# Kernel tuning notes

Hardware: AMD Instinct MI355X
Metric: run time of the kernel (lower is better)

The kernel has to match this reference:

```python
import jax, jax.numpy as jnp
import numpy as np

HIDDEN = 2048
INTER = 1408
N_ROUTED = 32
N_SHARED = 2
TOP_K = 6
B, S = 2, 1024


def setup_inputs() -> dict:
    key = jax.random.key(0)
    ks = jax.random.split(key, 9)
    scale = 0.02
    x = jax.random.normal(ks[0], (B, S, HIDDEN), dtype=jnp.float32)
    w_router = jax.random.normal(ks[1], (HIDDEN, N_ROUTED), dtype=jnp.float32) * scale
    wg = jax.random.normal(ks[2], (N_ROUTED, HIDDEN, INTER), dtype=jnp.float32) * scale
    wu = jax.random.normal(ks[3], (N_ROUTED, HIDDEN, INTER), dtype=jnp.float32) * scale
    wd = jax.random.normal(ks[4], (N_ROUTED, INTER, HIDDEN), dtype=jnp.float32) * scale
    sg = jax.random.normal(ks[5], (N_SHARED, HIDDEN, INTER), dtype=jnp.float32) * scale
    su = jax.random.normal(ks[6], (N_SHARED, HIDDEN, INTER), dtype=jnp.float32) * scale
    sd = jax.random.normal(ks[7], (N_SHARED, INTER, HIDDEN), dtype=jnp.float32) * scale
    return {"x": x, "w_router": w_router, "wg": wg, "wu": wu, "wd": wd,
            "sg": sg, "su": su, "sd": sd}


def _swiglu(xf, wg_e, wu_e, wd_e):
    # xf: [T, D]; wg_e/wu_e: [D, F]; wd_e: [F, D]
    h = jax.nn.silu(xf @ wg_e) * (xf @ wu_e)
    return h @ wd_e


def reference(x, w_router, wg, wu, wd, sg, su, sd):
    Bb, Ss, D = x.shape
    xf = x.reshape(-1, D)                      # [T, D], T = B*S
    T = xf.shape[0]

    # Shared experts: applied densely to every token, summed.
    shared = jnp.zeros_like(xf)
    for i in range(sg.shape[0]):               # small fixed count (2)
        shared = shared + _swiglu(xf, sg[i], su[i], sd[i])

    # Router: softmax over all routed experts, then top-k + renormalize.
    probs = jax.nn.softmax(xf @ w_router, axis=-1)            # [T, E]
    topw, topi = jax.lax.top_k(probs, TOP_K)                  # [T, K]
    topw = topw / jnp.sum(topw, axis=-1, keepdims=True)

    # Dense [T, E] combine weights (zero where expert not selected).
    E = wg.shape[0]
    wdense = jnp.zeros((T, E), dtype=xf.dtype)
    wdense = wdense.at[jnp.arange(T)[:, None], topi].add(topw)

    # Scan over experts, accumulating weighted expert outputs (memory-light).
    def body(acc, ew):
        wg_e, wu_e, wd_e, w_e = ew            # w_e: [T] combine weight for this expert
        y = _swiglu(xf, wg_e, wu_e, wd_e)     # [T, D]
        return acc + w_e[:, None] * y, None

    routed, _ = jax.lax.scan(body, jnp.zeros_like(xf), (wg, wu, wd, wdense.T))

    return (shared + routed).reshape(Bb, Ss, D)
```

## Files before the change

### kernel.cpp

```cpp
#include <hip/hip_runtime.h>
#include <hip/hip_bf16.h>

#define T_TOK 2048
#define D_HID 2048
#define F_INT 1408
#define N_EXP 32
#define TOPK 6
#define NJOBS 34
#define SH_BASE 12288
#define ROWS_TOTAL 16384
#define MAXT_GU 159
#define GU_NBN 22
#define MAXT_DN 159
#define LDSW 40

typedef __bf16 bf16;
typedef __bf16 bf16x4 __attribute__((ext_vector_type(4)));
typedef __bf16 bf16x8 __attribute__((ext_vector_type(8)));
typedef float f32x4 __attribute__((ext_vector_type(4)));

#define BAR() asm volatile("s_waitcnt lgkmcnt(0)\n\ts_barrier" ::: "memory")

__device__ __forceinline__ int swz16(int r, int k) {
    return r * LDSW + ((((k >> 3) ^ ((r >> 3) & 3) ^ ((r >> 5) & 3)) & 3) << 3) + (k & 7);
}

__device__ __forceinline__ int decode_tile(const int* __restrict__ counts, int bid,
                                           int NBN, int MSH, int NSH,
                                           int& job, int& n0, int& m0) {
    int total = 0;
    for (int j = 0; j < NJOBS; ++j) {
        int c = (j < N_EXP) ? counts[j] : T_TOK;
        total += ((c + (1 << MSH) - 1) >> MSH) * NBN;
    }
    if (bid >= total) return 0;
    int q = total >> 3, r = total & 7, x = bid & 7, o = bid >> 3;
    int L = (x < r ? x * (q + 1) : r * (q + 1) + (x - r) * q) + o;
    int acc = 0;
    for (int j = 0; j < NJOBS; ++j) {
        int c = (j < N_EXP) ? counts[j] : T_TOK;
        int tc = (c + (1 << MSH) - 1) >> MSH;
        int b = tc * NBN;
        if (L < acc + b) {
            int rem = L - acc;
            int n0i = rem / tc;
            job = j;
            n0 = n0i << NSH;
            m0 = (rem - n0i * tc) << MSH;
            return 1;
        }
        acc += b;
    }
    return 0;
}

__global__ __launch_bounds__(256) void k_xcvt(const float* __restrict__ x,
                                              bf16* __restrict__ xb) {
    int i = blockIdx.x * 2048 + threadIdx.x * 8;
    float4 f0 = *(const float4*)(x + i);
    float4 f1 = *(const float4*)(x + i + 4);
    bf16x8 v = {(bf16)f0.x, (bf16)f0.y, (bf16)f0.z, (bf16)f0.w,
                (bf16)f1.x, (bf16)f1.y, (bf16)f1.z, (bf16)f1.w};
    *(bf16x8*)(xb + i) = v;
}

__global__ __launch_bounds__(256) void k_router(const float* __restrict__ x,
                                                const float* __restrict__ wr,
                                                int* __restrict__ counts,
                                                int* __restrict__ tok_e,
                                                float* __restrict__ tok_w) {
    int t = blockIdx.x;
    int tid = threadIdx.x;
    __shared__ float xs[D_HID];
    __shared__ float part[8][32];
    __shared__ float probs[N_EXP];

    const float4* xsrc = (const float4*)(x + (size_t)t * D_HID);
    float4* xdst = (float4*)xs;
    for (int i = tid; i < D_HID / 4; i += 256) xdst[i] = xsrc[i];
    __syncthreads();

    int e = tid & 31, c = tid >> 5;
    float p = 0.f;
    const float* wp = wr + e;
    #pragma unroll 8
    for (int h = c * 256; h < c * 256 + 256; ++h) p += xs[h] * wp[h * 32];
    part[c][e] = p;
    __syncthreads();

    if (tid < 32) {
        float l = 0.f;
        #pragma unroll
        for (int cc = 0; cc < 8; ++cc) l += part[cc][tid];
        float m = l;
        for (int off = 16; off; off >>= 1) m = fmaxf(m, __shfl_xor(m, off));
        float ex = __expf(l - m);
        float s = ex;
        for (int off = 16; off; off >>= 1) s += __shfl_xor(s, off);
        probs[tid] = ex / s;
    }
    __syncthreads();

    if (tid == 0) {
        unsigned used = 0;
        int ids[TOPK]; float wsv[TOPK]; float wsum = 0.f;
        for (int k = 0; k < TOPK; ++k) {
            int best = 0; float bv = -1.f;
            for (int ee = 0; ee < N_EXP; ++ee)
                if (!((used >> ee) & 1u) && probs[ee] > bv) { bv = probs[ee]; best = ee; }
            used |= 1u << best;
            ids[k] = best; wsv[k] = bv; wsum += bv;
        }
        float inv = 1.f / wsum;
        for (int k = 0; k < TOPK; ++k) {
            tok_e[t * TOPK + k] = ids[k];
            tok_w[t * TOPK + k] = wsv[k] * inv;
            atomicAdd(&counts[ids[k]], 1);
        }
    }
}

__global__ void k_plan(const int* __restrict__ counts, int* __restrict__ offs,
                       int* __restrict__ cursors) {
    int tid = threadIdx.x;
    if (tid < N_EXP) cursors[tid] = 0;
    if (tid == 0) {
        int o = 0;
        offs[0] = 0;
        for (int e2 = 0; e2 < N_EXP; ++e2) { o += counts[e2]; offs[e2 + 1] = o; }
        offs[33] = offs[32] + T_TOK;
        offs[34] = offs[33] + T_TOK;
    }
}

__global__ __launch_bounds__(256) void k_assign(const int* __restrict__ tok_e,
                                                const int* __restrict__ offs,
                                                int* __restrict__ cursors,
                                                int* __restrict__ slots,
                                                int* __restrict__ rowtok) {
    int t = blockIdx.x * 256 + threadIdx.x;
    #pragma unroll
    for (int k = 0; k < TOPK; ++k) {
        int e = tok_e[t * TOPK + k];
        int pos = atomicAdd(&cursors[e], 1);
        int slot = offs[e] + pos;
        slots[t * TOPK + k] = slot;
        rowtok[slot] = t;
    }
    rowtok[SH_BASE + t] = t;
    rowtok[SH_BASE + T_TOK + t] = t;
}

__global__ __launch_bounds__(256, 3) void k_gateup(
    const bf16* __restrict__ xb, const float* __restrict__ wg, const float* __restrict__ wu,
    const float* __restrict__ sg, const float* __restrict__ su,
    const int* __restrict__ rowtok, const int* __restrict__ counts, const int* __restrict__ offs,
    bf16* __restrict__ H) {

    int job, n0, m0;
    if (!decode_tile(counts, blockIdx.x, GU_NBN, 7, 6, job, n0, m0)) return;
    int cnt = (job < N_EXP) ? counts[job] : T_TOK;
    int base = offs[job];
    const float* Wg = (job < N_EXP) ? wg + (size_t)job * D_HID * F_INT
                                    : sg + (size_t)(job - N_EXP) * D_HID * F_INT;
    const float* Wu = (job < N_EXP) ? wu + (size_t)job * D_HID * F_INT
                                    : su + (size_t)(job - N_EXP) * D_HID * F_INT;

    __shared__ bf16 As[2][128 * LDSW];
    __shared__ bf16 Bg[2][64 * LDSW];
    __shared__ bf16 Bu[2][64 * LDSW];

    int tid = threadIdx.x;
    int lane = tid & 63;
    int wid = tid >> 6;
    int wm = (wid & 1) * 64;
    int wn = (wid >> 1) * 32;

    int ar = tid >> 1;
    int akg2 = (tid & 1) * 2;
    int grow_a = m0 + ar; if (grow_a > cnt - 1) grow_a = cnt - 1;
    const bf16* asrc = xb + (size_t)rowtok[base + grow_a] * D_HID + akg2 * 8;

    int sub = tid & 127;
    int k4 = (sub & 7) * 4;
    int nn = (sub >> 3) * 4;
    const float* wsrc = ((tid & 128) ? Wu : Wg) + (size_t)k4 * F_INT + n0 + nn;

    f32x4 accg[4][2], accu[4][2];
    f32x4 zero = {0.f, 0.f, 0.f, 0.f};
    #pragma unroll
    for (int i = 0; i < 4; ++i)
        #pragma unroll
        for (int j = 0; j < 2; ++j) { accg[i][j] = zero; accu[i][j] = zero; }

    bf16x8 a_r[2];
    float4 b_r[4];

    auto LOAD = [&](int k0) {
        a_r[0] = *(const bf16x8*)(asrc + k0);
        a_r[1] = *(const bf16x8*)(asrc + k0 + 8);
        const float* b0 = wsrc + (size_t)k0 * F_INT;
        b_r[0] = *(const float4*)b0;
        b_r[1] = *(const float4*)(b0 + F_INT);
        b_r[2] = *(const float4*)(b0 + 2 * F_INT);
        b_r[3] = *(const float4*)(b0 + 3 * F_INT);
    };

    auto WRITE = [&](int s) {
        *(bf16x8*)&As[s][swz16(ar, akg2 * 8)] = a_r[0];
        *(bf16x8*)&As[s][swz16(ar, (akg2 + 1) * 8)] = a_r[1];
        bf16* bd = (tid & 128) ? Bu[s] : Bg[s];
        bf16x4 p0 = {(bf16)b_r[0].x, (bf16)b_r[1].x, (bf16)b_r[2].x, (bf16)b_r[3].x};
        bf16x4 p1 = {(bf16)b_r[0].y, (bf16)b_r[1].y, (bf16)b_r[2].y, (bf16)b_r[3].y};
        bf16x4 p2 = {(bf16)b_r[0].z, (bf16)b_r[1].z, (bf16)b_r[2].z, (bf16)b_r[3].z};
        bf16x4 p3 = {(bf16)b_r[0].w, (bf16)b_r[1].w, (bf16)b_r[2].w, (bf16)b_r[3].w};
        *(bf16x4*)&bd[swz16(nn + 0, k4)] = p0;
        *(bf16x4*)&bd[swz16(nn + 1, k4)] = p1;
        *(bf16x4*)&bd[swz16(nn + 2, k4)] = p2;
        *(bf16x4*)&bd[swz16(nn + 3, k4)] = p3;
    };

    const int NT = D_HID / 32;
    LOAD(0);
    WRITE(0);
    LOAD(32);
    BAR();

    for (int kt = 0; kt < NT; ++kt) {
        int cur = kt & 1;
        if (kt + 1 < NT) WRITE(cur ^ 1);
        if (kt + 2 < NT) LOAD((kt + 2) * 32);

        int kgl = (lane >> 4) * 8;
        bf16x8 af[4];
        #pragma unroll
        for (int mf = 0; mf < 4; ++mf)
            af[mf] = *(const bf16x8*)&As[cur][swz16(wm + mf * 16 + (lane & 15), kgl)];
        #pragma unroll
        for (int nf = 0; nf < 2; ++nf) {
            int rn = wn + nf * 16 + (lane & 15);
            int o = swz16(rn, kgl);
            bf16x8 bfr = *(const bf16x8*)&Bg[cur][o];
            bf16x8 ufr = *(const bf16x8*)&Bu[cur][o];
            #pragma unroll
            for (int mf = 0; mf < 4; ++mf) {
                accg[mf][nf] = __builtin_amdgcn_mfma_f32_16x16x32_bf16(af[mf], bfr, accg[mf][nf], 0, 0, 0);
                accu[mf][nf] = __builtin_amdgcn_mfma_f32_16x16x32_bf16(af[mf], ufr, accu[mf][nf], 0, 0, 0);
            }
        }
        BAR();
    }

    #pragma unroll
    for (int mf = 0; mf < 4; ++mf) {
        #pragma unroll
        for (int nf = 0; nf < 2; ++nf) {
            int col = n0 + wn + nf * 16 + (lane & 15);
            #pragma unroll
            for (int r = 0; r < 4; ++r) {
                int grow = m0 + wm + mf * 16 + (lane >> 4) * 4 + r;
                if (grow < cnt) {
                    float g = accg[mf][nf][r];
                    float u = accu[mf][nf][r];
                    float h = g * u / (1.f + __expf(-g));
                    H[(size_t)(base + grow) * F_INT + col] = (bf16)h;
                }
            }
        }
    }
}

__global__ __launch_bounds__(256, 3) void k_down(
    const bf16* __restrict__ H, const float* __restrict__ wd, const float* __restrict__ sd,
    const int* __restrict__ counts, const int* __restrict__ offs,
    bf16* __restrict__ P) {

    int job, n0, m0;
    if (!decode_tile(counts, blockIdx.x, D_HID / 128, 7, 7, job, n0, m0)) return;
    int cnt = (job < N_EXP) ? counts[job] : T_TOK;
    int base = offs[job];
    const float* Wd = (job < N_EXP) ? wd + (size_t)job * F_INT * D_HID
                                    : sd + (size_t)(job - N_EXP) * F_INT * D_HID;

    __shared__ bf16 As[2][128 * LDSW];
    __shared__ bf16 Bs[2][128 * LDSW];

    int tid = threadIdx.x;
    int lane = tid & 63;
    int wid = tid >> 6;
    int wm = (wid >> 1) * 64;
    int wn = (wid & 1) * 64;

    int ar = tid >> 1;
    int akg2 = (tid & 1) * 2;
    int grow_a = m0 + ar; if (grow_a > cnt - 1) grow_a = cnt - 1;
    const bf16* asrc = H + (size_t)(base + grow_a) * F_INT + akg2 * 8;

    int k4 = (tid >> 5) * 4;
    int nn = (tid & 31) * 4;
    const float* bsrc = Wd + (size_t)k4 * D_HID + n0 + nn;

    f32x4 acc[4][4];
    f32x4 zero = {0.f, 0.f, 0.f, 0.f};
    #pragma unroll
    for (int i = 0; i < 4; ++i)
        #pragma unroll
        for (int j = 0; j < 4; ++j) acc[i][j] = zero;

    bf16x8 h_r[2];
    float4 b_r[4];

    auto LOAD = [&](int k0) {
        h_r[0] = *(const bf16x8*)(asrc + k0);
        h_r[1] = *(const bf16x8*)(asrc + k0 + 8);
        const float* b0 = bsrc + (size_t)k0 * D_HID;
        b_r[0] = *(const float4*)b0;
        b_r[1] = *(const float4*)(b0 + D_HID);
        b_r[2] = *(const float4*)(b0 + 2 * D_HID);
        b_r[3] = *(const float4*)(b0 + 3 * D_HID);
    };

    auto WRITE = [&](int s) {
        *(bf16x8*)&As[s][swz16(ar, akg2 * 8)] = h_r[0];
        *(bf16x8*)&As[s][swz16(ar, (akg2 + 1) * 8)] = h_r[1];
        bf16x4 p0 = {(bf16)b_r[0].x, (bf16)b_r[1].x, (bf16)b_r[2].x, (bf16)b_r[3].x};
        bf16x4 p1 = {(bf16)b_r[0].y, (bf16)b_r[1].y, (bf16)b_r[2].y, (bf16)b_r[3].y};
        bf16x4 p2 = {(bf16)b_r[0].z, (bf16)b_r[1].z, (bf16)b_r[2].z, (bf16)b_r[3].z};
        bf16x4 p3 = {(bf16)b_r[0].w, (bf16)b_r[1].w, (bf16)b_r[2].w, (bf16)b_r[3].w};
        *(bf16x4*)&Bs[s][swz16(nn + 0, k4)] = p0;
        *(bf16x4*)&Bs[s][swz16(nn + 1, k4)] = p1;
        *(bf16x4*)&Bs[s][swz16(nn + 2, k4)] = p2;
        *(bf16x4*)&Bs[s][swz16(nn + 3, k4)] = p3;
    };

    const int NT = F_INT / 32;
    LOAD(0);
    WRITE(0);
    LOAD(32);
    BAR();

    for (int kt = 0; kt < NT; ++kt) {
        int cur = kt & 1;
        if (kt + 1 < NT) WRITE(cur ^ 1);
        if (kt + 2 < NT) LOAD((kt + 2) * 32);

        int kgl = (lane >> 4) * 8;
        bf16x8 af[4];
        #pragma unroll
        for (int mf = 0; mf < 4; ++mf)
            af[mf] = *(const bf16x8*)&As[cur][swz16(wm + mf * 16 + (lane & 15), kgl)];
        #pragma unroll
        for (int nf = 0; nf < 4; ++nf) {
            int rn = wn + nf * 16 + (lane & 15);
            bf16x8 bfr = *(const bf16x8*)&Bs[cur][swz16(rn, kgl)];
            #pragma unroll
            for (int mf = 0; mf < 4; ++mf)
                acc[mf][nf] = __builtin_amdgcn_mfma_f32_16x16x32_bf16(af[mf], bfr, acc[mf][nf], 0, 0, 0);
        }
        BAR();
    }

    #pragma unroll
    for (int mf = 0; mf < 4; ++mf) {
        #pragma unroll
        for (int nf = 0; nf < 4; ++nf) {
            int col = n0 + wn + nf * 16 + (lane & 15);
            #pragma unroll
            for (int r = 0; r < 4; ++r) {
                int grow = m0 + wm + mf * 16 + (lane >> 4) * 4 + r;
                if (grow < cnt)
                    P[(size_t)(base + grow) * D_HID + col] = (bf16)acc[mf][nf][r];
            }
        }
    }
}

__global__ __launch_bounds__(256) void k_combine(const bf16* __restrict__ P,
                                                 const int* __restrict__ slots,
                                                 const float* __restrict__ tok_w,
                                                 float* __restrict__ out) {
    int t = blockIdx.x;
    int tid = threadIdx.x;
    __shared__ int ss[TOPK];
    __shared__ float ww[TOPK];
    if (tid < TOPK) { ss[tid] = slots[t * TOPK + tid]; ww[tid] = tok_w[t * TOPK + tid]; }
    __syncthreads();
    int c0 = tid * 8;
    float acc[8];
    {
        bf16x8 v0 = *(const bf16x8*)(P + (size_t)(SH_BASE + t) * D_HID + c0);
        bf16x8 v1 = *(const bf16x8*)(P + (size_t)(SH_BASE + T_TOK + t) * D_HID + c0);
        #pragma unroll
        for (int i = 0; i < 8; ++i) acc[i] = (float)v0[i] + (float)v1[i];
    }
    #pragma unroll
    for (int k = 0; k < TOPK; ++k) {
        bf16x8 v = *(const bf16x8*)(P + (size_t)ss[k] * D_HID + c0);
        float w = ww[k];
        #pragma unroll
        for (int i = 0; i < 8; ++i) acc[i] += w * (float)v[i];
    }
    float4 o0 = {acc[0], acc[1], acc[2], acc[3]};
    float4 o1 = {acc[4], acc[5], acc[6], acc[7]};
    *(float4*)(out + (size_t)t * D_HID + c0) = o0;
    *(float4*)(out + (size_t)t * D_HID + c0 + 4) = o1;
}

extern "C" void kernel_launch(void* const* d_in, const int* in_sizes, int n_in,
                              void* d_out, int out_size, void* d_ws, size_t ws_size,
                              hipStream_t stream) {
    const float* x  = (const float*)d_in[0];
    const float* wr = (const float*)d_in[1];
    const float* wg = (const float*)d_in[2];
    const float* wu = (const float*)d_in[3];
    const float* wd = (const float*)d_in[4];
    const float* sg = (const float*)d_in[5];
    const float* su = (const float*)d_in[6];
    const float* sd = (const float*)d_in[7];
    float* out = (float*)d_out;

    char* w = (char*)d_ws;
    int*   counts   = (int*)(w + 0);
    int*   cursors  = (int*)(w + 256);
    int*   offs     = (int*)(w + 512);
    int*   tok_e    = (int*)(w + 8192);
    float* tok_w    = (float*)(w + 8192 + 49152);
    int*   slots    = (int*)(w + 8192 + 2 * 49152);
    int*   rowtok   = (int*)(w + 8192 + 3 * 49152);
    bf16*  H        = (bf16*)(w + 262144);
    bf16*  P        = (bf16*)(w + 262144 + (size_t)ROWS_TOTAL * F_INT * 2);
    bf16*  Xb       = (bf16*)(w + 262144 + (size_t)ROWS_TOTAL * F_INT * 2
                                        + (size_t)ROWS_TOTAL * D_HID * 2);

    hipMemsetAsync(counts, 0, 128, stream);
    k_xcvt<<<T_TOK * D_HID / 2048, 256, 0, stream>>>(x, Xb);
    k_router<<<T_TOK, 256, 0, stream>>>(x, wr, counts, tok_e, tok_w);
    k_plan<<<1, 64, 0, stream>>>(counts, offs, cursors);
    k_assign<<<T_TOK / 256, 256, 0, stream>>>(tok_e, offs, cursors, slots, rowtok);
    k_gateup<<<MAXT_GU * GU_NBN, 256, 0, stream>>>(
        Xb, wg, wu, sg, su, rowtok, counts, offs, H);
    k_down<<<MAXT_DN * (D_HID / 128), 256, 0, stream>>>(
        H, wd, sd, counts, offs, P);
    k_combine<<<T_TOK, 256, 0, stream>>>(P, slots, tok_w, out);
}
```

Baseline: 888.6 us.

## Pre-gather routed token rows and deepen weight prefetch in expert GEMMs

Adds a gather kernel that copies each routed and shared row of x into a contiguous bf16 buffer, so the gate/up GEMM reads A rows densely instead of through rowtok indirection. It falls back to the old per-token conversion when the workspace is too small. Both GEMM kernels now keep two register buffers of fp32 weights in flight, running the K loop two stages per iteration to hide global load latency. They also raise the launch-bounds occupancy hint from 3 to 4 blocks and change the B-load thread mapping so that more threads cover consecutive columns. The costs are extra register pressure, possible spills at the higher occupancy target, and the extra gather traffic of about 14K rows written and read back.

```diff
diff --git a/kernel.cpp b/kernel.cpp
--- a/kernel.cpp
+++ b/kernel.cpp
@@ -9,6 +9,7 @@
 #define NJOBS 34
 #define SH_BASE 12288
 #define ROWS_TOTAL 16384
+#define XP_ROWS 14336
 #define MAXT_GU 159
 #define GU_NBN 22
 #define MAXT_DN 159
@@ -54,16 +55,6 @@
     return 0;
 }
 
-__global__ __launch_bounds__(256) void k_xcvt(const float* __restrict__ x,
-                                              bf16* __restrict__ xb) {
-    int i = blockIdx.x * 2048 + threadIdx.x * 8;
-    float4 f0 = *(const float4*)(x + i);
-    float4 f1 = *(const float4*)(x + i + 4);
-    bf16x8 v = {(bf16)f0.x, (bf16)f0.y, (bf16)f0.z, (bf16)f0.w,
-                (bf16)f1.x, (bf16)f1.y, (bf16)f1.z, (bf16)f1.w};
-    *(bf16x8*)(xb + i) = v;
-}
-
 __global__ __launch_bounds__(256) void k_router(const float* __restrict__ x,
                                                 const float* __restrict__ wr,
                                                 int* __restrict__ counts,
@@ -151,11 +142,34 @@
     rowtok[SH_BASE + T_TOK + t] = t;
 }
 
-__global__ __launch_bounds__(256, 3) void k_gateup(
-    const bf16* __restrict__ xb, const float* __restrict__ wg, const float* __restrict__ wu,
+__global__ __launch_bounds__(256) void k_gather(const float* __restrict__ x,
+                                                const int* __restrict__ rowtok,
+                                                bf16* __restrict__ Xp) {
+    int s = blockIdx.x;
+    int src = (s < SH_BASE) ? rowtok[s] : (s - SH_BASE);
+    const float* xr = x + (size_t)src * D_HID + threadIdx.x * 8;
+    float4 f0 = *(const float4*)xr;
+    float4 f1 = *(const float4*)(xr + 4);
+    bf16x8 v = {(bf16)f0.x, (bf16)f0.y, (bf16)f0.z, (bf16)f0.w,
+                (bf16)f1.x, (bf16)f1.y, (bf16)f1.z, (bf16)f1.w};
+    *(bf16x8*)(Xp + (size_t)s * D_HID + threadIdx.x * 8) = v;
+}
+
+__global__ __launch_bounds__(256) void k_xcvt(const float* __restrict__ x,
+                                              bf16* __restrict__ xb) {
+    int i = blockIdx.x * 2048 + threadIdx.x * 8;
+    float4 f0 = *(const float4*)(x + i);
+    float4 f1 = *(const float4*)(x + i + 4);
+    bf16x8 v = {(bf16)f0.x, (bf16)f0.y, (bf16)f0.z, (bf16)f0.w,
+                (bf16)f1.x, (bf16)f1.y, (bf16)f1.z, (bf16)f1.w};
+    *(bf16x8*)(xb + i) = v;
+}
+
+__global__ __launch_bounds__(256, 4) void k_gateup(
+    const bf16* __restrict__ xp, const float* __restrict__ wg, const float* __restrict__ wu,
     const float* __restrict__ sg, const float* __restrict__ su,
     const int* __restrict__ rowtok, const int* __restrict__ counts, const int* __restrict__ offs,
-    bf16* __restrict__ H) {
+    bf16* __restrict__ H, int dense) {
 
     int job, n0, m0;
     if (!decode_tile(counts, blockIdx.x, GU_NBN, 7, 6, job, n0, m0)) return;
@@ -179,11 +193,13 @@
     int ar = tid >> 1;
     int akg2 = (tid & 1) * 2;
     int grow_a = m0 + ar; if (grow_a > cnt - 1) grow_a = cnt - 1;
-    const bf16* asrc = xb + (size_t)rowtok[base + grow_a] * D_HID + akg2 * 8;
+    int arow = dense ? (((job < N_EXP) ? base : SH_BASE) + grow_a)
+                     : rowtok[base + grow_a];
+    const bf16* asrc = xp + (size_t)arow * D_HID + akg2 * 8;
 
     int sub = tid & 127;
-    int k4 = (sub & 7) * 4;
-    int nn = (sub >> 3) * 4;
+    int nn = (sub & 15) * 4;
+    int k4 = (sub >> 4) * 4;
     const float* wsrc = ((tid & 128) ? Wu : Wg) + (size_t)k4 * F_INT + n0 + nn;
 
     f32x4 accg[4][2], accu[4][2];
@@ -194,43 +210,33 @@
         for (int j = 0; j < 2; ++j) { accg[i][j] = zero; accu[i][j] = zero; }
 
     bf16x8 a_r[2];
-    float4 b_r[4];
-
-    auto LOAD = [&](int k0) {
+    float4 rb0[4], rb1[4];
+
+    auto LOADA = [&](int k0) {
         a_r[0] = *(const bf16x8*)(asrc + k0);
         a_r[1] = *(const bf16x8*)(asrc + k0 + 8);
+    };
+    auto LOADB = [&](float4 (&rb)[4], int k0) {
         const float* b0 = wsrc + (size_t)k0 * F_INT;
-        b_r[0] = *(const float4*)b0;
-        b_r[1] = *(const float4*)(b0 + F_INT);
-        b_r[2] = *(const float4*)(b0 + 2 * F_INT);
-        b_r[3] = *(const float4*)(b0 + 3 * F_INT);
-    };
-
-    auto WRITE = [&](int s) {
+        rb[0] = *(const float4*)b0;
+        rb[1] = *(const float4*)(b0 + F_INT);
+        rb[2] = *(const float4*)(b0 + 2 * F_INT);
+        rb[3] = *(const float4*)(b0 + 3 * F_INT);
+    };
+    auto WRITE = [&](int s, float4 (&rb)[4]) {
         *(bf16x8*)&As[s][swz16(ar, akg2 * 8)] = a_r[0];
         *(bf16x8*)&As[s][swz16(ar, (akg2 + 1) * 8)] = a_r[1];
         bf16* bd = (tid & 128) ? Bu[s] : Bg[s];
-        bf16x4 p0 = {(bf16)b_r[0].x, (bf16)b_r[1].x, (bf16)b_r[2].x, (bf16)b_r[3].x};
-        bf16x4 p1 = {(bf16)b_r[0].y, (bf16)b_r[1].y, (bf16)b_r[2].y, (bf16)b_r[3].y};
-        bf16x4 p2 = {(bf16)b_r[0].z, (bf16)b_r[1].z, (bf16)b_r[2].z, (bf16)b_r[3].z};
-        bf16x4 p3 = {(bf16)b_r[0].w, (bf16)b_r[1].w, (bf16)b_r[2].w, (bf16)b_r[3].w};
+        bf16x4 p0 = {(bf16)rb[0].x, (bf16)rb[1].x, (bf16)rb[2].x, (bf16)rb[3].x};
+        bf16x4 p1 = {(bf16)rb[0].y, (bf16)rb[1].y, (bf16)rb[2].y, (bf16)rb[3].y};
+        bf16x4 p2 = {(bf16)rb[0].z, (bf16)rb[1].z, (bf16)rb[2].z, (bf16)rb[3].z};
+        bf16x4 p3 = {(bf16)rb[0].w, (bf16)rb[1].w, (bf16)rb[2].w, (bf16)rb[3].w};
         *(bf16x4*)&bd[swz16(nn + 0, k4)] = p0;
         *(bf16x4*)&bd[swz16(nn + 1, k4)] = p1;
         *(bf16x4*)&bd[swz16(nn + 2, k4)] = p2;
         *(bf16x4*)&bd[swz16(nn + 3, k4)] = p3;
     };
-
-    const int NT = D_HID / 32;
-    LOAD(0);
-    WRITE(0);
-    LOAD(32);
-    BAR();
-
-    for (int kt = 0; kt < NT; ++kt) {
-        int cur = kt & 1;
-        if (kt + 1 < NT) WRITE(cur ^ 1);
-        if (kt + 2 < NT) LOAD((kt + 2) * 32);
-
+    auto MM = [&](int cur) {
         int kgl = (lane >> 4) * 8;
         bf16x8 af[4];
         #pragma unroll
@@ -238,8 +244,7 @@
             af[mf] = *(const bf16x8*)&As[cur][swz16(wm + mf * 16 + (lane & 15), kgl)];
         #pragma unroll
         for (int nf = 0; nf < 2; ++nf) {
-            int rn = wn + nf * 16 + (lane & 15);
-            int o = swz16(rn, kgl);
+            int o = swz16(wn + nf * 16 + (lane & 15), kgl);
             bf16x8 bfr = *(const bf16x8*)&Bg[cur][o];
             bf16x8 ufr = *(const bf16x8*)&Bu[cur][o];
             #pragma unroll
@@ -248,6 +253,24 @@
                 accu[mf][nf] = __builtin_amdgcn_mfma_f32_16x16x32_bf16(af[mf], ufr, accu[mf][nf], 0, 0, 0);
             }
         }
+    };
+
+    const int NT = D_HID / 32;
+    LOADB(rb0, 0); LOADB(rb1, 32); LOADA(0);
+    WRITE(0, rb0);
+    LOADA(32); LOADB(rb0, 64);
+    BAR();
+
+    for (int kt = 0; kt < NT; kt += 2) {
+        if (kt + 1 < NT) WRITE(1, rb1);
+        if (kt + 2 < NT) LOADA((kt + 2) * 32);
+        if (kt + 3 < NT) LOADB(rb1, (kt + 3) * 32);
+        MM(0);
+        BAR();
+        if (kt + 2 < NT) WRITE(0, rb0);
+        if (kt + 3 < NT) LOADA((kt + 3) * 32);
+        if (kt + 4 < NT) LOADB(rb0, (kt + 4) * 32);
+        MM(1);
         BAR();
     }
 
@@ -270,7 +293,7 @@
     }
 }
 
-__global__ __launch_bounds__(256, 3) void k_down(
+__global__ __launch_bounds__(256, 4) void k_down(
     const bf16* __restrict__ H, const float* __restrict__ wd, const float* __restrict__ sd,
     const int* __restrict__ counts, const int* __restrict__ offs,
     bf16* __restrict__ P) {
@@ -308,42 +331,32 @@
         for (int j = 0; j < 4; ++j) acc[i][j] = zero;
 
     bf16x8 h_r[2];
-    float4 b_r[4];
-
-    auto LOAD = [&](int k0) {
+    float4 rb0[4], rb1[4];
+
+    auto LOADA = [&](int k0) {
         h_r[0] = *(const bf16x8*)(asrc + k0);
         h_r[1] = *(const bf16x8*)(asrc + k0 + 8);
+    };
+    auto LOADB = [&](float4 (&rb)[4], int k0) {
         const float* b0 = bsrc + (size_t)k0 * D_HID;
-        b_r[0] = *(const float4*)b0;
-        b_r[1] = *(const float4*)(b0 + D_HID);
-        b_r[2] = *(const float4*)(b0 + 2 * D_HID);
-        b_r[3] = *(const float4*)(b0 + 3 * D_HID);
-    };
-
-    auto WRITE = [&](int s) {
+        rb[0] = *(const float4*)b0;
+        rb[1] = *(const float4*)(b0 + D_HID);
+        rb[2] = *(const float4*)(b0 + 2 * D_HID);
+        rb[3] = *(const float4*)(b0 + 3 * D_HID);
+    };
+    auto WRITE = [&](int s, float4 (&rb)[4]) {
         *(bf16x8*)&As[s][swz16(ar, akg2 * 8)] = h_r[0];
         *(bf16x8*)&As[s][swz16(ar, (akg2 + 1) * 8)] = h_r[1];
-        bf16x4 p0 = {(bf16)b_r[0].x, (bf16)b_r[1].x, (bf16)b_r[2].x, (bf16)b_r[3].x};
-        bf16x4 p1 = {(bf16)b_r[0].y, (bf16)b_r[1].y, (bf16)b_r[2].y, (bf16)b_r[3].y};
-        bf16x4 p2 = {(bf16)b_r[0].z, (bf16)b_r[1].z, (bf16)b_r[2].z, (bf16)b_r[3].z};
-        bf16x4 p3 = {(bf16)b_r[0].w, (bf16)b_r[1].w, (bf16)b_r[2].w, (bf16)b_r[3].w};
+        bf16x4 p0 = {(bf16)rb[0].x, (bf16)rb[1].x, (bf16)rb[2].x, (bf16)rb[3].x};
+        bf16x4 p1 = {(bf16)rb[0].y, (bf16)rb[1].y, (bf16)rb[2].y, (bf16)rb[3].y};
+        bf16x4 p2 = {(bf16)rb[0].z, (bf16)rb[1].z, (bf16)rb[2].z, (bf16)rb[3].z};
+        bf16x4 p3 = {(bf16)rb[0].w, (bf16)rb[1].w, (bf16)rb[2].w, (bf16)rb[3].w};
         *(bf16x4*)&Bs[s][swz16(nn + 0, k4)] = p0;
         *(bf16x4*)&Bs[s][swz16(nn + 1, k4)] = p1;
         *(bf16x4*)&Bs[s][swz16(nn + 2, k4)] = p2;
         *(bf16x4*)&Bs[s][swz16(nn + 3, k4)] = p3;
     };
-
-    const int NT = F_INT / 32;
-    LOAD(0);
-    WRITE(0);
-    LOAD(32);
-    BAR();
-
-    for (int kt = 0; kt < NT; ++kt) {
-        int cur = kt & 1;
-        if (kt + 1 < NT) WRITE(cur ^ 1);
-        if (kt + 2 < NT) LOAD((kt + 2) * 32);
-
+    auto MM = [&](int cur) {
         int kgl = (lane >> 4) * 8;
         bf16x8 af[4];
         #pragma unroll
@@ -351,12 +364,29 @@
             af[mf] = *(const bf16x8*)&As[cur][swz16(wm + mf * 16 + (lane & 15), kgl)];
         #pragma unroll
         for (int nf = 0; nf < 4; ++nf) {
-            int rn = wn + nf * 16 + (lane & 15);
-            bf16x8 bfr = *(const bf16x8*)&Bs[cur][swz16(rn, kgl)];
+            bf16x8 bfr = *(const bf16x8*)&Bs[cur][swz16(wn + nf * 16 + (lane & 15), kgl)];
             #pragma unroll
             for (int mf = 0; mf < 4; ++mf)
                 acc[mf][nf] = __builtin_amdgcn_mfma_f32_16x16x32_bf16(af[mf], bfr, acc[mf][nf], 0, 0, 0);
         }
+    };
+
+    const int NT = F_INT / 32;
+    LOADB(rb0, 0); LOADB(rb1, 32); LOADA(0);
+    WRITE(0, rb0);
+    LOADA(32); LOADB(rb0, 64);
+    BAR();
+
+    for (int kt = 0; kt < NT; kt += 2) {
+        if (kt + 1 < NT) WRITE(1, rb1);
+        if (kt + 2 < NT) LOADA((kt + 2) * 32);
+        if (kt + 3 < NT) LOADB(rb1, (kt + 3) * 32);
+        MM(0);
+        BAR();
+        if (kt + 2 < NT) WRITE(0, rb0);
+        if (kt + 3 < NT) LOADA((kt + 3) * 32);
+        if (kt + 4 < NT) LOADB(rb0, (kt + 4) * 32);
+        MM(1);
         BAR();
     }
 
@@ -419,6 +449,10 @@
     const float* sd = (const float*)d_in[7];
     float* out = (float*)d_out;
 
+    const size_t H_BYTES  = (size_t)ROWS_TOTAL * F_INT * 2;
+    const size_t P_BYTES  = (size_t)ROWS_TOTAL * D_HID * 2;
+    const size_t XP_BYTES = (size_t)XP_ROWS * D_HID * 2;
+
     char* w = (char*)d_ws;
     int*   counts   = (int*)(w + 0);
     int*   cursors  = (int*)(w + 256);
@@ -428,17 +462,22 @@
     int*   slots    = (int*)(w + 8192 + 2 * 49152);
     int*   rowtok   = (int*)(w + 8192 + 3 * 49152);
     bf16*  H        = (bf16*)(w + 262144);
-    bf16*  P        = (bf16*)(w + 262144 + (size_t)ROWS_TOTAL * F_INT * 2);
-    bf16*  Xb       = (bf16*)(w + 262144 + (size_t)ROWS_TOTAL * F_INT * 2
-                                        + (size_t)ROWS_TOTAL * D_HID * 2);
+    bf16*  P        = (bf16*)(w + 262144 + H_BYTES);
+    bf16*  Xp       = (bf16*)(w + 262144 + H_BYTES + P_BYTES);
+
+    int dense = (ws_size >= 262144 + H_BYTES + P_BYTES + XP_BYTES) ? 1 : 0;
 
     hipMemsetAsync(counts, 0, 128, stream);
-    k_xcvt<<<T_TOK * D_HID / 2048, 256, 0, stream>>>(x, Xb);
     k_router<<<T_TOK, 256, 0, stream>>>(x, wr, counts, tok_e, tok_w);
     k_plan<<<1, 64, 0, stream>>>(counts, offs, cursors);
     k_assign<<<T_TOK / 256, 256, 0, stream>>>(tok_e, offs, cursors, slots, rowtok);
+    if (dense) {
+        k_gather<<<XP_ROWS, 256, 0, stream>>>(x, rowtok, Xp);
+    } else {
+        k_xcvt<<<T_TOK * D_HID / 2048, 256, 0, stream>>>(x, Xp);
+    }
     k_gateup<<<MAXT_GU * GU_NBN, 256, 0, stream>>>(
-        Xb, wg, wu, sg, su, rowtok, counts, offs, H);
+        Xp, wg, wu, sg, su, rowtok, counts, offs, H, dense);
     k_down<<<MAXT_DN * (D_HID / 128), 256, 0, stream>>>(
         H, wd, sd, counts, offs, P);
     k_combine<<<T_TOK, 256, 0, stream>>>(P, slots, tok_w, out);
```

Result: slower. 1.656 ms (+86.4%).
